# Kernel optimization log

Measured on AMD Instinct MI355X. Metric: run time of the kernel, lower is better.

## Reference

```python
import jax, jax.numpy as jnp
import numpy as np

EMB = 256
HID = 512
VOCAB = 32000
SRC_LEN = 50
TRG_LEN = 50
BATCH = 64


def lstm_layer(x, h0, c0, Wih, Whh, b):
    """x: [T,B,in]; h0,c0: [B,H]; Wih: [4H,in]; Whh: [4H,H]; b: [4H].
    PyTorch gate order i,f,g,o. Returns (ys [T,B,H], hT, cT)."""
    def step(carry, xt):
        h, c = carry
        g = xt @ Wih.T + h @ Whh.T + b
        i, f, gg, o = jnp.split(g, 4, axis=-1)
        c = jax.nn.sigmoid(f) * c + jax.nn.sigmoid(i) * jnp.tanh(gg)
        h = jax.nn.sigmoid(o) * jnp.tanh(c)
        return (h, c), h
    (hT, cT), ys = jax.lax.scan(step, (h0, c0), x)
    return ys, hT, cT


def setup_inputs() -> dict:
    key = jax.random.key(0)
    ks = jax.random.split(key, 20)
    s = 0.05
    d = {
        'src': jax.random.randint(ks[0], (SRC_LEN, BATCH), 0, VOCAB),
        'trg': jax.random.randint(ks[1], (TRG_LEN, BATCH), 0, VOCAB),
        'enc_emb': jax.random.normal(ks[2], (VOCAB, EMB), jnp.float32) * s,
        'enc_Wih0': jax.random.normal(ks[3], (4 * HID, EMB), jnp.float32) * s,
        'enc_Whh0': jax.random.normal(ks[4], (4 * HID, HID), jnp.float32) * s,
        'enc_b0': jnp.zeros((4 * HID,), jnp.float32),
        'enc_Wih1': jax.random.normal(ks[5], (4 * HID, HID), jnp.float32) * s,
        'enc_Whh1': jax.random.normal(ks[6], (4 * HID, HID), jnp.float32) * s,
        'enc_b1': jnp.zeros((4 * HID,), jnp.float32),
        'dec_emb': jax.random.normal(ks[7], (VOCAB, EMB), jnp.float32) * s,
        'dec_Wih0': jax.random.normal(ks[8], (4 * HID, EMB), jnp.float32) * s,
        'dec_Whh0': jax.random.normal(ks[9], (4 * HID, HID), jnp.float32) * s,
        'dec_b0': jnp.zeros((4 * HID,), jnp.float32),
        'dec_Wih1': jax.random.normal(ks[10], (4 * HID, HID), jnp.float32) * s,
        'dec_Whh1': jax.random.normal(ks[11], (4 * HID, HID), jnp.float32) * s,
        'dec_b1': jnp.zeros((4 * HID,), jnp.float32),
        'out_W': jax.random.normal(ks[12], (VOCAB, HID), jnp.float32) * s,
        'out_b': jnp.zeros((VOCAB,), jnp.float32),
    }
    return d


def reference(src, trg, enc_emb, enc_Wih0, enc_Whh0, enc_b0, enc_Wih1, enc_Whh1,
              enc_b1, dec_emb, dec_Wih0, dec_Whh0, dec_b0, dec_Wih1, dec_Whh1,
              dec_b1, out_W, out_b):
    B = src.shape[1]
    z = jnp.zeros((B, HID), enc_emb.dtype)
    # Encoder: 2-layer LSTM over src, keep final (h, c) per layer
    xe = enc_emb[src]                                   # [S,B,E]
    y0, h0, c0 = lstm_layer(xe, z, z, enc_Wih0, enc_Whh0, enc_b0)
    _, h1, c1 = lstm_layer(y0, z, z, enc_Wih1, enc_Whh1, enc_b1)
    # Decoder with teacher forcing: inputs are trg[0:T-1]
    xd = dec_emb[trg[:-1]]                              # [T-1,B,E]
    d0, _, _ = lstm_layer(xd, h0, c0, dec_Wih0, dec_Whh0, dec_b0)
    d1, _, _ = lstm_layer(d0, h1, c1, dec_Wih1, dec_Whh1, dec_b1)
    preds = d1 @ out_W.T + out_b                        # [T-1,B,V]
    return preds
```

## Files before the change

### kernel.cpp

```cpp
#include <hip/hip_runtime.h>
#include <hip/hip_bf16.h>

#define BATCH 64
#define HID 512
#define EMB 256
#define VOCAB 32000
#define G4 2048

typedef __attribute__((ext_vector_type(8))) short short8;
typedef __attribute__((ext_vector_type(4))) float f32x4;
typedef __attribute__((ext_vector_type(4))) unsigned short ush4;

__global__ __launch_bounds__(256) void zero_kernel(float* p, int n){
    int i = blockIdx.x*256 + threadIdx.x;
    if (i < n) p[i] = 0.f;
}

__device__ __forceinline__ unsigned short bf16_rne(float x){
    unsigned b = __float_as_uint(x);
    return (unsigned short)((b + 0x7fffu + ((b >> 16) & 1u)) >> 16);
}
__device__ __forceinline__ void split2(float x, unsigned short& h, unsigned short& l){
    h = bf16_rne(x);
    l = bf16_rne(x - __uint_as_float((unsigned)h << 16));
}

__global__ __launch_bounds__(256) void embed_kernel(const int* __restrict__ tok,
                                                    const float* __restrict__ emb,
                                                    float* __restrict__ out, int T){
    int i = blockIdx.x*256 + threadIdx.x;
    int n = T*BATCH*(EMB/4);
    if (i >= n) return;
    int e4 = i % (EMB/4);
    int tb = i / (EMB/4);
    int id = tok[tb];
    reinterpret_cast<float4*>(out)[(size_t)tb*(EMB/4) + e4] =
        reinterpret_cast<const float4*>(emb + (size_t)id*EMB)[e4];
}

__global__ __launch_bounds__(256) void embed_plane_kernel(const int* __restrict__ tok,
                                                          const float* __restrict__ emb,
                                                          unsigned short* __restrict__ hi,
                                                          unsigned short* __restrict__ lo, int T){
    int i = blockIdx.x*256 + threadIdx.x;
    int n = T*BATCH*(EMB/4);
    if (i >= n) return;
    int e4 = i % (EMB/4);
    int tb = i / (EMB/4);
    int id = tok[tb];
    f32x4 v = reinterpret_cast<const f32x4*>(emb + (size_t)id*EMB)[e4];
    ush4 h, l;
    #pragma unroll
    for (int j = 0; j < 4; j++){ unsigned short a,b; split2(v[j], a, b); h[j]=a; l[j]=b; }
    reinterpret_cast<ush4*>(hi)[(size_t)tb*(EMB/4) + e4] = h;
    reinterpret_cast<ush4*>(lo)[(size_t)tb*(EMB/4) + e4] = l;
}

__global__ __launch_bounds__(256) void split_kernel(const float* __restrict__ in,
                                                    unsigned short* __restrict__ hi,
                                                    unsigned short* __restrict__ lo, int n4){
    int i = blockIdx.x*256 + threadIdx.x;
    if (i >= n4) return;
    f32x4 v = reinterpret_cast<const f32x4*>(in)[i];
    ush4 h, l;
    #pragma unroll
    for (int j = 0; j < 4; j++){ unsigned short a,b; split2(v[j], a, b); h[j]=a; l[j]=b; }
    reinterpret_cast<ush4*>(hi)[i] = h;
    reinterpret_cast<ush4*>(lo)[i] = l;
}

__global__ __launch_bounds__(256) void split_all_kernel(
    const float* __restrict__ outW, unsigned short* __restrict__ Whi,
    const float* __restrict__ w0, unsigned short* __restrict__ w0h, unsigned short* __restrict__ w0l,
    const float* __restrict__ w1, unsigned short* __restrict__ w1h, unsigned short* __restrict__ w1l,
    const float* __restrict__ w2, unsigned short* __restrict__ w2h, unsigned short* __restrict__ w2l,
    const float* __restrict__ w3, unsigned short* __restrict__ w3h, unsigned short* __restrict__ w3l)
{
    int i = blockIdx.x*256 + threadIdx.x;
    if (i < 4096000){
        f32x4 v = reinterpret_cast<const f32x4*>(outW)[i];
        ush4 h;
        #pragma unroll
        for (int j = 0; j < 4; j++) h[j] = bf16_rne(v[j]);
        reinterpret_cast<ush4*>(Whi)[i] = h;
        return;
    }
    i -= 4096000;
    const float* src; unsigned short* dh; unsigned short* dl;
    if (i < 131072){ src = w0; dh = w0h; dl = w0l; }
    else if (i < 131072+262144){ i -= 131072; src = w1; dh = w1h; dl = w1l; }
    else if (i < 131072+262144+131072){ i -= 131072+262144; src = w2; dh = w2h; dl = w2l; }
    else if (i < 131072+262144+131072+262144){ i -= 131072+262144+131072; src = w3; dh = w3h; dl = w3l; }
    else return;
    f32x4 v = reinterpret_cast<const f32x4*>(src)[i];
    ush4 h, l;
    #pragma unroll
    for (int j = 0; j < 4; j++){ unsigned short a,b; split2(v[j], a, b); h[j]=a; l[j]=b; }
    reinterpret_cast<ush4*>(dh)[i] = h;
    reinterpret_cast<ush4*>(dl)[i] = l;
}

template<int KDIM, int NDIM>
__global__ __launch_bounds__(256) void gemm_mfma_split(
    const float* __restrict__ A, const float* __restrict__ B,
    const float* __restrict__ bias, float* __restrict__ C, int M)
{
    constexpr int LS = 40;
    __shared__ unsigned short Ah[128*LS], Al[128*LS], Bh[128*LS], Bl[128*LS];
    const int n0 = blockIdx.x*128, m0 = blockIdx.y*128;
    const int tid  = threadIdx.x;
    const int lane = tid & 63, wid = tid >> 6;
    const int wm = wid >> 1, wn = wid & 1;
    const int srow = tid >> 1, sk = (tid & 1)*16;
    f32x4 acc[4][4] = {};

    for (int k0 = 0; k0 < KDIM; k0 += 32){
        __syncthreads();
        {
            int ar = m0 + srow;
            float xv[16];
            if (ar < M){
                const float4* ap = reinterpret_cast<const float4*>(A + (size_t)ar*KDIM + k0 + sk);
                #pragma unroll
                for (int q = 0; q < 4; q++){
                    float4 v = ap[q];
                    xv[q*4+0]=v.x; xv[q*4+1]=v.y; xv[q*4+2]=v.z; xv[q*4+3]=v.w;
                }
            } else {
                #pragma unroll
                for (int q = 0; q < 16; q++) xv[q] = 0.f;
            }
            #pragma unroll
            for (int q = 0; q < 16; q++){
                unsigned short h,l; split2(xv[q], h, l);
                Ah[srow*LS + sk + q] = h;
                Al[srow*LS + sk + q] = l;
            }
        }
        {
            int br = n0 + srow;
            const float4* bp = reinterpret_cast<const float4*>(B + (size_t)br*KDIM + k0 + sk);
            #pragma unroll
            for (int q = 0; q < 4; q++){
                float4 v = bp[q];
                float xs[4] = {v.x, v.y, v.z, v.w};
                #pragma unroll
                for (int j = 0; j < 4; j++){
                    unsigned short h,l; split2(xs[j], h, l);
                    Bh[srow*LS + sk + q*4 + j] = h;
                    Bl[srow*LS + sk + q*4 + j] = l;
                }
            }
        }
        __syncthreads();
        const int fr = lane & 15, fk = (lane >> 4)*8;
        short8 a_h[4], a_l[4], b_h[4], b_l[4];
        #pragma unroll
        for (int mi = 0; mi < 4; mi++){
            int row = wm*64 + mi*16 + fr;
            a_h[mi] = *reinterpret_cast<const short8*>(&Ah[row*LS + fk]);
            a_l[mi] = *reinterpret_cast<const short8*>(&Al[row*LS + fk]);
        }
        #pragma unroll
        for (int nj = 0; nj < 4; nj++){
            int rowb = wn*64 + nj*16 + fr;
            b_h[nj] = *reinterpret_cast<const short8*>(&Bh[rowb*LS + fk]);
            b_l[nj] = *reinterpret_cast<const short8*>(&Bl[rowb*LS + fk]);
        }
        #pragma unroll
        for (int mi = 0; mi < 4; mi++)
            #pragma unroll
            for (int nj = 0; nj < 4; nj++){
                acc[mi][nj] = __builtin_amdgcn_mfma_f32_16x16x32_bf16(a_h[mi], b_h[nj], acc[mi][nj], 0,0,0);
                acc[mi][nj] = __builtin_amdgcn_mfma_f32_16x16x32_bf16(a_h[mi], b_l[nj], acc[mi][nj], 0,0,0);
                acc[mi][nj] = __builtin_amdgcn_mfma_f32_16x16x32_bf16(a_l[mi], b_h[nj], acc[mi][nj], 0,0,0);
            }
    }
    const int fr = lane & 15, fq = lane >> 4;
    #pragma unroll
    for (int nj = 0; nj < 4; nj++){
        int col = n0 + wn*64 + nj*16 + fr;
        float bv = bias[col];
        #pragma unroll
        for (int mi = 0; mi < 4; mi++){
            int rbase = m0 + wm*64 + mi*16 + fq*4;
            #pragma unroll
            for (int j = 0; j < 4; j++){
                int row = rbase + j;
                if (row < M)
                    __builtin_nontemporal_store(acc[mi][nj][j] + bv, &C[(size_t)row*NDIM + col]);
            }
        }
    }
}

__device__ __forceinline__ void gll16(const unsigned short* g, unsigned short* l){
    __builtin_amdgcn_global_load_lds(
        (const __attribute__((address_space(1))) unsigned int*)g,
        (__attribute__((address_space(3))) unsigned int*)l, 16, 0, 0);
}

template<int KDIM, int NDIM, int NTN>
__device__ __forceinline__ void gemm_gll_body(
    const unsigned short* __restrict__ Ahi, const unsigned short* __restrict__ Alo,
    const unsigned short* __restrict__ Bhi, const unsigned short* __restrict__ Blo,
    const float* __restrict__ bias, float* __restrict__ C, int M,
    int bid_raw, int total)
{
    __shared__ unsigned short P[4][128*32];
    const int q = total >> 3, r8 = total & 7;
    const int xcd = bid_raw & 7, idx = bid_raw >> 3;
    const int lid = (xcd < r8 ? xcd*(q+1) : r8*(q+1) + (xcd - r8)*q) + idx;
    const int m0 = (lid / NTN)*128, n0 = (lid % NTN)*128;

    const int tid  = threadIdx.x;
    const int lane = tid & 63, wid = tid >> 6;
    const int wm = wid >> 1, wn = wid & 1;

    const unsigned short* gsrc = (wid == 0) ? Ahi : (wid == 1) ? Alo
                               : (wid == 2) ? Bhi : Blo;
    const int row0 = (wid < 2) ? m0 : n0;
    const unsigned short* gbase = gsrc + (size_t)(row0 + (lane >> 2))*KDIM
                                       + 8*((lane & 3) ^ ((lane >> 3) & 3));
    unsigned short* lbase = &P[wid][0];

    f32x4 acc[4][4] = {};

    for (int k0 = 0; k0 < KDIM; k0 += 32){
        __syncthreads();
        #pragma unroll
        for (int i = 0; i < 8; i++)
            gll16(gbase + k0 + (size_t)i*16*KDIM, lbase + i*512);
        __syncthreads();

        const int fr = lane & 15, fkq = lane >> 4;
        const int swz = 8*(fkq ^ ((fr >> 1) & 3));
        short8 a_h[4], a_l[4], b_h[4], b_l[4];
        #pragma unroll
        for (int mi = 0; mi < 4; mi++){
            int row = wm*64 + mi*16 + fr;
            a_h[mi] = *reinterpret_cast<const short8*>(&P[0][row*32 + swz]);
            a_l[mi] = *reinterpret_cast<const short8*>(&P[1][row*32 + swz]);
        }
        #pragma unroll
        for (int nj = 0; nj < 4; nj++){
            int row = wn*64 + nj*16 + fr;
            b_h[nj] = *reinterpret_cast<const short8*>(&P[2][row*32 + swz]);
            b_l[nj] = *reinterpret_cast<const short8*>(&P[3][row*32 + swz]);
        }
        #pragma unroll
        for (int mi = 0; mi < 4; mi++)
            #pragma unroll
            for (int nj = 0; nj < 4; nj++){
                acc[mi][nj] = __builtin_amdgcn_mfma_f32_16x16x32_bf16(a_h[mi], b_h[nj], acc[mi][nj], 0,0,0);
                acc[mi][nj] = __builtin_amdgcn_mfma_f32_16x16x32_bf16(a_l[mi], b_h[nj], acc[mi][nj], 0,0,0);
                acc[mi][nj] = __builtin_amdgcn_mfma_f32_16x16x32_bf16(a_h[mi], b_l[nj], acc[mi][nj], 0,0,0);
            }
    }
    const int fr = lane & 15, fq = lane >> 4;
    #pragma unroll
    for (int nj = 0; nj < 4; nj++){
        int col = n0 + wn*64 + nj*16 + fr;
        float bv = bias[col];
        #pragma unroll
        for (int mi = 0; mi < 4; mi++){
            int rbase = m0 + wm*64 + mi*16 + fq*4;
            #pragma unroll
            for (int j = 0; j < 4; j++){
                int row = rbase + j;
                if (row < M)
                    __builtin_nontemporal_store(acc[mi][nj][j] + bv, &C[(size_t)row*NDIM + col]);
            }
        }
    }
}

template<int KDIM, int NDIM, int NTN>
__global__ __launch_bounds__(256) void gemm_planes_gll(
    const unsigned short* Ahi, const unsigned short* Alo,
    const unsigned short* Bhi, const unsigned short* Blo,
    const float* bias, float* C, int M)
{
    gemm_gll_body<KDIM, NDIM, NTN>(Ahi, Alo, Bhi, Blo, bias, C, M,
                                   blockIdx.x, gridDim.x);
}

template<int KDIM, int NDIM, int NTN>
__global__ __launch_bounds__(512) void gemm_planes_256w8(
    const unsigned short* __restrict__ Ahi,
    const unsigned short* __restrict__ Bhi,
    const float* __restrict__ bias, float* __restrict__ C, int M)
{
    __shared__ unsigned short Ah[256*32];
    __shared__ unsigned short Bh[128*32];
    const int total = gridDim.x;
    const int q = total >> 3, r8 = total & 7;
    const int xcd = blockIdx.x & 7, idx = blockIdx.x >> 3;
    const int lid = (xcd < r8 ? xcd*(q+1) : r8*(q+1) + (xcd - r8)*q) + idx;
    const int m0 = (lid / NTN)*256, n0 = (lid % NTN)*128;

    const int tid  = threadIdx.x;
    const int lane = tid & 63, wid = tid >> 6;
    const int wm = wid >> 1, wn = wid & 1;

    const bool stager = (wid < 6);
    const unsigned short* gsrc = (wid < 4) ? Ahi : Bhi;
    const int grow0 = (wid < 4) ? (m0 + wid*64) : (n0 + (wid - 4)*64);
    const unsigned short* gbase = gsrc + (size_t)(grow0 + (lane >> 2))*KDIM
                                       + 8*((lane & 3) ^ ((lane >> 3) & 3));
    unsigned short* lbase = (wid < 4) ? (Ah + wid*64*32) : (Bh + (wid - 4)*64*32);

    f32x4 acc[4][4] = {};

    for (int k0 = 0; k0 < KDIM; k0 += 32){
        __syncthreads();
        if (stager){
            #pragma unroll
            for (int i = 0; i < 4; i++)
                gll16(gbase + k0 + (size_t)i*16*KDIM, lbase + i*512);
        }
        __syncthreads();

        const int fr = lane & 15, fkq = lane >> 4;
        const int swz = 8*(fkq ^ ((fr >> 1) & 3));
        short8 a_h[4], b_h[4];
        #pragma unroll
        for (int nj = 0; nj < 4; nj++){
            int row = wn*64 + nj*16 + fr;
            b_h[nj] = *reinterpret_cast<const short8*>(&Bh[row*32 + swz]);
        }
        #pragma unroll
        for (int mi = 0; mi < 4; mi++){
            int row = wm*64 + mi*16 + fr;
            a_h[mi] = *reinterpret_cast<const short8*>(&Ah[row*32 + swz]);
        }
        #pragma unroll
        for (int mi = 0; mi < 4; mi++)
            #pragma unroll
            for (int nj = 0; nj < 4; nj++)
                acc[mi][nj] = __builtin_amdgcn_mfma_f32_16x16x32_bf16(a_h[mi], b_h[nj], acc[mi][nj], 0,0,0);
    }
    const int fr = lane & 15, fq = lane >> 4;
    #pragma unroll
    for (int nj = 0; nj < 4; nj++){
        int col = n0 + wn*64 + nj*16 + fr;
        float bv = bias[col];
        #pragma unroll
        for (int mi = 0; mi < 4; mi++){
            int rbase = m0 + wm*64 + mi*16 + fq*4;
            #pragma unroll
            for (int j = 0; j < 4; j++){
                int row = rbase + j;
                if (row < M)
                    __builtin_nontemporal_store(acc[mi][nj][j] + bv, &C[(size_t)row*NDIM + col]);
            }
        }
    }
}

__device__ __forceinline__ void lstm_body(
    const float* __restrict__ Xp, const float* __restrict__ Whh,
    const float* __restrict__ hinit, const float* __restrict__ cinit,
    float* __restrict__ ys, float* __restrict__ cfin,
    int T, unsigned* __restrict__ flagbase, int bx,
    unsigned short* __restrict__ phi, unsigned short* __restrict__ plo)
{
    constexpr int WS = 520;
    __shared__ unsigned short hH[8*WS], hL[8*WS];
    __shared__ __align__(16) float red[4*544 + 128];
    __shared__ unsigned short zbuf[8];

    const int bc  = bx & 7, hc = bx >> 3;
    const int hid0 = hc*16;
    const int tid = threadIdx.x;
    const int lane = tid & 63, kc = tid >> 6;
    const int fr = lane & 15, fkq = lane >> 4;
    unsigned* myflag = flagbase + (size_t)(bc*32 + hc)*16;

    if (tid < 8) zbuf[tid] = 0;

    short8 ah[4][4], al[4][4];
    #pragma unroll
    for (int m = 0; m < 4; m++){
        const float* wr = Whh + (size_t)(m*HID + hid0 + fr)*HID;
        #pragma unroll
        for (int s = 0; s < 4; s++){
            int k0 = kc*128 + s*32 + fkq*8;
            f32x4 v0 = *reinterpret_cast<const f32x4*>(wr + k0);
            f32x4 v1 = *reinterpret_cast<const f32x4*>(wr + k0 + 4);
            short8 h8, l8;
            float xv[8] = {v0[0],v0[1],v0[2],v0[3],v1[0],v1[1],v1[2],v1[3]};
            #pragma unroll
            for (int j = 0; j < 8; j++){
                unsigned short hh, ll; split2(xv[j], hh, ll);
                h8[j] = (short)hh; l8[j] = (short)ll;
            }
            ah[m][s] = h8; al[m][s] = l8;
        }
    }

    const int ub = tid >> 4;
    const int uh = tid & 15;
    float creg = 0.f;
    if (tid < 128) creg = cinit[(size_t)(bc*8 + ub)*HID + hid0 + uh];

    const size_t hbase = (size_t)bc*8*HID;
    const float* xprow = Xp + (size_t)(bc*8 + ub)*G4 + hid0 + uh;

    float xn0=0.f, xn1=0.f, xn2=0.f, xn3=0.f;
    if (tid < 128){
        const float* xpr = xprow;
        xn0 = xpr[0]; xn1 = xpr[512]; xn2 = xpr[1024]; xn3 = xpr[1536];
    }

    for (int t = 0; t < T; t++){
        {
            const f32x4* hsrc = reinterpret_cast<const f32x4*>(
                (t == 0) ? (hinit + hbase) : (ys + (size_t)(t-1)*BATCH*HID + hbase));
            #pragma unroll
            for (int j = 0; j < 4; j++){
                int fidx = tid + j*256;
                f32x4 v = hsrc[fidx];
                int e   = fidx*4;
                int row = e >> 9, col = e & 511;
                ush4 h, l;
                #pragma unroll
                for (int qq = 0; qq < 4; qq++){ unsigned short a,b; split2(v[qq], a, b); h[qq]=a; l[qq]=b; }
                *reinterpret_cast<ush4*>(&hH[row*WS + col]) = h;
                *reinterpret_cast<ush4*>(&hL[row*WS + col]) = l;
            }
        }
        __syncthreads();

        {
            f32x4 acc4[4] = {};
            const bool breal = fr < 8;
            #pragma unroll
            for (int s = 0; s < 4; s++){
                int k0 = kc*128 + s*32 + fkq*8;
                short8 bh = breal ? *reinterpret_cast<const short8*>(&hH[fr*WS + k0])
                                  : *reinterpret_cast<const short8*>(zbuf);
                short8 bl = breal ? *reinterpret_cast<const short8*>(&hL[fr*WS + k0])
                                  : *reinterpret_cast<const short8*>(zbuf);
                #pragma unroll
                for (int m = 0; m < 4; m++){
                    acc4[m] = __builtin_amdgcn_mfma_f32_16x16x32_bf16(ah[m][s], bh, acc4[m], 0,0,0);
                    acc4[m] = __builtin_amdgcn_mfma_f32_16x16x32_bf16(ah[m][s], bl, acc4[m], 0,0,0);
                    acc4[m] = __builtin_amdgcn_mfma_f32_16x16x32_bf16(al[m][s], bh, acc4[m], 0,0,0);
                }
            }
            const int b = lane & 15;
            if (b < 8){
                #pragma unroll
                for (int m = 0; m < 4; m++)
                    *reinterpret_cast<f32x4*>(&red[kc*544 + b*68 + m*16 + (lane >> 4)*4]) = acc4[m];
            }
        }
        __syncthreads();

        if (tid < 64){
            #pragma unroll
            for (int b = 0; b < 8; b++)
                red[b*68 + tid] = red[b*68 + tid] + red[544 + b*68 + tid]
                               + red[1088 + b*68 + tid] + red[1632 + b*68 + tid];
        }
        __syncthreads();

        if (tid < 128){
            float gi = red[ub*68 + 0*16 + uh] + xn0;
            float gf = red[ub*68 + 1*16 + uh] + xn1;
            float gg = red[ub*68 + 2*16 + uh] + xn2;
            float go = red[ub*68 + 3*16 + uh] + xn3;
            float si = 1.f/(1.f + expf(-gi));
            float sf = 1.f/(1.f + expf(-gf));
            float so = 1.f/(1.f + expf(-go));
            float tg = tanhf(gg);
            float c = sf*creg + si*tg;
            creg = c;
            float hval = so * tanhf(c);
            red[2176 + tid] = hval;
            if (phi){
                unsigned short hh, ll; split2(hval, hh, ll);
                size_t poff = (size_t)t*BATCH*HID + (size_t)(bc*8 + ub)*HID + hid0 + uh;
                phi[poff] = hh; plo[poff] = ll;
            }
            if (t < T-1){
                const float* xpr = xprow + (size_t)(t+1)*BATCH*G4;
                xn0 = xpr[0]; xn1 = xpr[512]; xn2 = xpr[1024]; xn3 = xpr[1536];
            }
        }
        __syncthreads();

        if (tid < 64){
            if (tid < 32){
                f32x4 v = *reinterpret_cast<const f32x4*>(&red[2176 + tid*4]);
                const f32x4* addr = reinterpret_cast<const f32x4*>(
                    ys + (size_t)t*BATCH*HID
                       + (size_t)(bc*8 + (tid >> 2))*HID + hid0 + (tid & 3)*4);
                asm volatile("global_store_dwordx4 %0, %1, off sc0 sc1"
                             :: "v"(addr), "v"(v) : "memory");
            }
            if (t < T-1){
                asm volatile("s_waitcnt vmcnt(0)" ::: "memory");
                if (tid == 0)
                    __hip_atomic_store(myflag, (unsigned)(t+1),
                                       __ATOMIC_RELAXED, __HIP_MEMORY_SCOPE_AGENT);
                const unsigned tgt = (unsigned)(t+1);
                unsigned* fp = flagbase + (size_t)(bc*32 + (tid & 31))*16;
                unsigned spins = 0;
                bool done = false;
                while (!done && spins < (1u<<20)){
                    unsigned v = tgt;
                    if (tid < 32)
                        v = __hip_atomic_load(fp, __ATOMIC_RELAXED, __HIP_MEMORY_SCOPE_AGENT);
                    done = (bool)__all((int)(v >= tgt));
                    spins++;
                }
            }
        }
        __syncthreads();
    }

    if (tid < 128)
        cfin[(size_t)(bc*8 + ub)*HID + hid0 + uh] = creg;
}

__global__ __launch_bounds__(256, 2) void lstm_layer_k(
    const float* Xp, const float* Whh, const float* hinit, const float* cinit,
    float* ys, float* cfin, int T, unsigned* flagbase,
    unsigned short* phi, unsigned short* plo)
{
    lstm_body(Xp, Whh, hinit, cinit, ys, cfin, T, flagbase, blockIdx.x, phi, plo);
}

__global__ __launch_bounds__(256, 2) void lstm_dual_k(
    const float* Xp0, const float* Whh0, const float* hi0, const float* ci0,
    float* ys0, float* cf0, int T0, unsigned* fl0,
    unsigned short* phi0, unsigned short* plo0,
    const float* Xp1, const float* Whh1, const float* hi1, const float* ci1,
    float* ys1, float* cf1, int T1, unsigned* fl1,
    unsigned short* phi1, unsigned short* plo1)
{
    const int role = blockIdx.x >> 8;
    const int bx = blockIdx.x & 255;
    if (role == 0)
        lstm_body(Xp0, Whh0, hi0, ci0, ys0, cf0, T0, fl0, bx, phi0, plo0);
    else
        lstm_body(Xp1, Whh1, hi1, ci1, ys1, cf1, T1, fl1, bx, phi1, plo1);
}

__global__ __launch_bounds__(256, 2) void lstm_gemm_k(
    const float* Xp, const float* Whh, const float* hinit, const float* cinit,
    float* ys, float* cfin, int T, unsigned* flagbase,
    unsigned short* phi, unsigned short* plo,
    const unsigned short* gAhi, const unsigned short* gAlo,
    const unsigned short* gBhi, const unsigned short* gBlo,
    const float* gbias, float* gC, int gM, int gTotal)
{
    if ((int)blockIdx.x < 256)
        lstm_body(Xp, Whh, hinit, cinit, ys, cfin, T, flagbase, blockIdx.x, phi, plo);
    else
        gemm_gll_body<EMB, G4, 16>(gAhi, gAlo, gBhi, gBlo, gbias, gC, gM,
                                   blockIdx.x - 256, gTotal);
}

extern "C" void kernel_launch(void* const* d_in, const int* in_sizes, int n_in,
                              void* d_out, int out_size, void* d_ws, size_t ws_size,
                              hipStream_t stream) {
    const int*   src      = (const int*)  d_in[0];
    const int*   trg      = (const int*)  d_in[1];
    const float* enc_emb  = (const float*)d_in[2];
    const float* enc_Wih0 = (const float*)d_in[3];
    const float* enc_Whh0 = (const float*)d_in[4];
    const float* enc_b0   = (const float*)d_in[5];
    const float* enc_Wih1 = (const float*)d_in[6];
    const float* enc_Whh1 = (const float*)d_in[7];
    const float* enc_b1   = (const float*)d_in[8];
    const float* dec_emb  = (const float*)d_in[9];
    const float* dec_Wih0 = (const float*)d_in[10];
    const float* dec_Whh0 = (const float*)d_in[11];
    const float* dec_b0   = (const float*)d_in[12];
    const float* dec_Wih1 = (const float*)d_in[13];
    const float* dec_Whh1 = (const float*)d_in[14];
    const float* dec_b1   = (const float*)d_in[15];
    const float* out_W    = (const float*)d_in[16];
    const float* out_b    = (const float*)d_in[17];

    float* ob = (float*)d_out;
    float* Xp   = ob;
    float* xe   = ob + (size_t)6553600;
    float* xd   = ob + (size_t)7372800;
    float* eys0 = ob + (size_t)8175616;
    float* eys1 = ob + (size_t)9814016;
    float* dys0 = ob + (size_t)11452416;
    float* Xp2  = ob + (size_t)13058048;

    float* ws = (float*)d_ws;
    float* dys1 = ws;
    float* c0   = ws + (size_t)1605632;
    float* c1   = ws + (size_t)1638400;
    float* hz   = ws + (size_t)1671168;
    unsigned* flags = (unsigned*)(ws + (size_t)1703936);
    unsigned short* Whi = (unsigned short*)(ws + (size_t)1720320);
    unsigned short* Wlo = Whi + (size_t)16384000;
    unsigned short* Ahi = Wlo + (size_t)16384000;
    unsigned short* Alo = Ahi + (size_t)1703936;
    unsigned short* eW0h = Alo  + (size_t)1703936;
    unsigned short* eW0l = eW0h + (size_t)524288;
    unsigned short* eW1h = eW0l + (size_t)524288;
    unsigned short* eW1l = eW1h + (size_t)1048576;
    unsigned short* dW0h = eW1l + (size_t)1048576;
    unsigned short* dW0l = dW0h + (size_t)524288;
    unsigned short* dW1h = dW0l + (size_t)524288;
    unsigned short* dW1l = dW1h + (size_t)1048576;
    unsigned short* XAh  = dW1l + (size_t)1048576;
    unsigned short* XAl  = XAh  + (size_t)1638400;
    const size_t end_xp = (size_t)1720320*4 +
        2*((size_t)16384000*2 + (size_t)1703936*2 + (size_t)524288*4 +
           (size_t)1048576*4 + (size_t)1638400*2);
    const bool xp_ok = (ws_size >= end_xp);

    {
        int n = 3*BATCH*HID + 4*4096;
        zero_kernel<<<(n+255)/256, 256, 0, stream>>>(c0, n);
    }

    if (xp_ok){
        split_all_kernel<<<(4882432 + 255)/256, 256, 0, stream>>>(
            out_W, Whi,
            enc_Wih0, eW0h, eW0l,  enc_Wih1, eW1h, eW1l,
            dec_Wih0, dW0h, dW0l,  dec_Wih1, dW1h, dW1l);
        embed_plane_kernel<<<(50*BATCH*(EMB/4)+255)/256, 256, 0, stream>>>(src, enc_emb, XAh, XAl, 50);
        embed_plane_kernel<<<(49*BATCH*(EMB/4)+255)/256, 256, 0, stream>>>(trg, dec_emb, Ahi, Alo, 49);
    } else {
        embed_kernel<<<(50*BATCH*(EMB/4)+255)/256, 256, 0, stream>>>(src, enc_emb, xe, 50);
        embed_kernel<<<(49*BATCH*(EMB/4)+255)/256, 256, 0, stream>>>(trg, dec_emb, xd, 49);
    }

    dim3 xgrid(G4/128, 25);

    if (xp_ok)
        gemm_planes_gll<EMB, G4, 16><<<400, 256, 0, stream>>>(XAh, XAl, eW0h, eW0l, enc_b0, Xp, 3200);
    else
        gemm_mfma_split<EMB, G4><<<xgrid, 256, 0, stream>>>(xe, enc_Wih0, enc_b0, Xp, 3200);

    if (xp_ok){
        lstm_gemm_k<<<656, 256, 0, stream>>>(
            Xp, enc_Whh0, hz, hz, eys0, c0, 50, flags + 0, XAh, XAl,
            Ahi, Alo, dW0h, dW0l, dec_b0, Xp2, 3136, 400);
    } else {
        lstm_layer_k<<<256, 256, 0, stream>>>(Xp, enc_Whh0, hz, hz, eys0, c0, 50, flags + 0,
                                              nullptr, nullptr);
        gemm_mfma_split<EMB, G4><<<xgrid, 256, 0, stream>>>(xd, dec_Wih0, dec_b0, Xp2, 3136);
    }

    if (xp_ok)
        gemm_planes_gll<HID, G4, 16><<<400, 256, 0, stream>>>(XAh, XAl, eW1h, eW1l, enc_b1, Xp, 3200);
    else
        gemm_mfma_split<HID, G4><<<xgrid, 256, 0, stream>>>(eys0, enc_Wih1, enc_b1, Xp, 3200);

    lstm_dual_k<<<512, 256, 0, stream>>>(
        Xp,  enc_Whh1, hz,                          hz, eys1, c1, 50, flags + 4096,  nullptr, nullptr,
        Xp2, dec_Whh0, eys0 + (size_t)49*BATCH*HID, c0, dys0, c0, 49, flags + 8192,
        xp_ok ? XAh : nullptr, XAl);

    if (xp_ok)
        gemm_planes_gll<HID, G4, 16><<<400, 256, 0, stream>>>(XAh, XAl, dW1h, dW1l, dec_b1, Xp, 3136);
    else
        gemm_mfma_split<HID, G4><<<xgrid, 256, 0, stream>>>(dys0, dec_Wih1, dec_b1, Xp, 3136);
    lstm_layer_k<<<256, 256, 0, stream>>>(Xp, dec_Whh1, eys1 + (size_t)49*BATCH*HID, c1,
                                          dys1, c1, 49, flags + 12288,
                                          xp_ok ? Ahi : nullptr, Alo);

    if (xp_ok){
        gemm_planes_256w8<HID, VOCAB, 250><<<13*250, 512, 0, stream>>>(
            Ahi, Whi, out_b, (float*)d_out, 3136);
    } else {
        gemm_mfma_split<HID, VOCAB><<<dim3(VOCAB/128, 25), 256, 0, stream>>>(
            dys1, out_W, out_b, (float*)d_out, 3136);
    }
}
```

Measured before the change: 945.8 us.

## Fuse final decoder LSTM layer with vocab projection GEMM via progress flags

Merges the last decoder LSTM layer and the output vocabulary GEMM into one persistent launch. LSTM blocks publish per-batch-chunk progress counters, and GEMM blocks spin-wait until the time steps covering their row tile are done, so the large projection overlaps the serial recurrence. A 512-thread LSTM body variant is added, and the decoder layer-1 input projection gets its own workspace buffer so it does not alias. This relies on co-residency of the LSTM blocks and uses bounded spin loops whose timeouts could break correctness if the GEMM blocks starve the LSTM blocks.

```diff
diff --git a/kernel.cpp b/kernel.cpp
--- a/kernel.cpp
+++ b/kernel.cpp
@@ -56,19 +56,6 @@
     reinterpret_cast<ush4*>(lo)[(size_t)tb*(EMB/4) + e4] = l;
 }
 
-__global__ __launch_bounds__(256) void split_kernel(const float* __restrict__ in,
-                                                    unsigned short* __restrict__ hi,
-                                                    unsigned short* __restrict__ lo, int n4){
-    int i = blockIdx.x*256 + threadIdx.x;
-    if (i >= n4) return;
-    f32x4 v = reinterpret_cast<const f32x4*>(in)[i];
-    ush4 h, l;
-    #pragma unroll
-    for (int j = 0; j < 4; j++){ unsigned short a,b; split2(v[j], a, b); h[j]=a; l[j]=b; }
-    reinterpret_cast<ush4*>(hi)[i] = h;
-    reinterpret_cast<ush4*>(lo)[i] = l;
-}
-
 __global__ __launch_bounds__(256) void split_all_kernel(
     const float* __restrict__ outW, unsigned short* __restrict__ Whi,
     const float* __restrict__ w0, unsigned short* __restrict__ w0h, unsigned short* __restrict__ w0l,
@@ -286,22 +273,39 @@
 }
 
 template<int KDIM, int NDIM, int NTN>
-__global__ __launch_bounds__(512) void gemm_planes_256w8(
+__device__ __forceinline__ void gemm_final_body(
     const unsigned short* __restrict__ Ahi,
     const unsigned short* __restrict__ Bhi,
-    const float* __restrict__ bias, float* __restrict__ C, int M)
+    const float* __restrict__ bias, float* __restrict__ C, int M,
+    int bid, int total, unsigned* __restrict__ gprog, int T)
 {
     __shared__ unsigned short Ah[256*32];
     __shared__ unsigned short Bh[128*32];
-    const int total = gridDim.x;
     const int q = total >> 3, r8 = total & 7;
-    const int xcd = blockIdx.x & 7, idx = blockIdx.x >> 3;
+    const int xcd = bid & 7, idx = bid >> 3;
     const int lid = (xcd < r8 ? xcd*(q+1) : r8*(q+1) + (xcd - r8)*q) + idx;
     const int m0 = (lid / NTN)*256, n0 = (lid % NTN)*128;
 
     const int tid  = threadIdx.x;
     const int lane = tid & 63, wid = tid >> 6;
     const int wm = wid >> 1, wn = wid & 1;
+
+    if (gprog){
+        int thresh = 4*(lid / NTN) + 4;
+        if (thresh > T) thresh = T;
+        if (tid < 64){
+            unsigned spins = 0; bool done = false;
+            while (!done && spins < (1u<<14)){
+                unsigned v = (unsigned)thresh;
+                if (tid < 8)
+                    v = __hip_atomic_load(&gprog[tid], __ATOMIC_RELAXED, __HIP_MEMORY_SCOPE_AGENT);
+                done = (bool)__all((int)(v >= (unsigned)thresh));
+                spins++;
+                if (!done) __builtin_amdgcn_s_sleep(8);
+            }
+        }
+        __syncthreads();
+    }
 
     const bool stager = (wid < 6);
     const unsigned short* gsrc = (wid < 4) ? Ahi : Bhi;
@@ -356,6 +360,15 @@
             }
         }
     }
+}
+
+template<int KDIM, int NDIM, int NTN>
+__global__ __launch_bounds__(512) void gemm_planes_256w8(
+    const unsigned short* Ahi, const unsigned short* Bhi,
+    const float* bias, float* C, int M)
+{
+    gemm_final_body<KDIM, NDIM, NTN>(Ahi, Bhi, bias, C, M,
+                                     blockIdx.x, gridDim.x, nullptr, 0);
 }
 
 __device__ __forceinline__ void lstm_body(
@@ -562,6 +575,217 @@
     else
         gemm_gll_body<EMB, G4, 16>(gAhi, gAlo, gBhi, gBlo, gbias, gC, gM,
                                    blockIdx.x - 256, gTotal);
+}
+
+__device__ __forceinline__ void lstm_body8(
+    const float* __restrict__ Xp, const float* __restrict__ Whh,
+    const float* __restrict__ hinit, const float* __restrict__ cinit,
+    float* __restrict__ ys, float* __restrict__ cfin,
+    int T, unsigned* __restrict__ flagbase, int bx,
+    unsigned short* __restrict__ phi, unsigned short* __restrict__ plo,
+    unsigned* __restrict__ gprog)
+{
+    constexpr int WS = 520;
+    __shared__ unsigned short hH[8*WS], hL[8*WS];
+    __shared__ __align__(16) float red[8*544 + 128];
+    __shared__ unsigned short zbuf[8];
+
+    const int bc = bx & 7, hc = bx >> 3;
+    const int hid0 = hc*16;
+    const int tid = threadIdx.x;
+    const int lane = tid & 63, kc = tid >> 6;
+    const int fr = lane & 15, fkq = lane >> 4;
+    unsigned* myflag = flagbase + (size_t)(bc*32 + hc)*16;
+
+    if (tid < 8) zbuf[tid] = 0;
+
+    short8 ah[4][2], al[4][2];
+    #pragma unroll
+    for (int m = 0; m < 4; m++){
+        const float* wr = Whh + (size_t)(m*HID + hid0 + fr)*HID;
+        #pragma unroll
+        for (int s = 0; s < 2; s++){
+            int k0 = kc*64 + s*32 + fkq*8;
+            f32x4 v0 = *reinterpret_cast<const f32x4*>(wr + k0);
+            f32x4 v1 = *reinterpret_cast<const f32x4*>(wr + k0 + 4);
+            short8 h8, l8;
+            float xv[8] = {v0[0],v0[1],v0[2],v0[3],v1[0],v1[1],v1[2],v1[3]};
+            #pragma unroll
+            for (int j = 0; j < 8; j++){
+                unsigned short hh, ll; split2(xv[j], hh, ll);
+                h8[j] = (short)hh; l8[j] = (short)ll;
+            }
+            ah[m][s] = h8; al[m][s] = l8;
+        }
+    }
+
+    const int ub = tid >> 4;
+    const int uh = tid & 15;
+    float creg = 0.f;
+    if (tid < 128) creg = cinit[(size_t)(bc*8 + ub)*HID + hid0 + uh];
+
+    const size_t hbase = (size_t)bc*8*HID;
+    const float* xprow = Xp + (size_t)(bc*8 + ub)*G4 + hid0 + uh;
+
+    float xn0=0.f, xn1=0.f, xn2=0.f, xn3=0.f;
+    if (tid < 128){
+        const float* xpr = xprow;
+        xn0 = xpr[0]; xn1 = xpr[512]; xn2 = xpr[1024]; xn3 = xpr[1536];
+    }
+
+    for (int t = 0; t < T; t++){
+        {
+            const f32x4* hsrc = reinterpret_cast<const f32x4*>(
+                (t == 0) ? (hinit + hbase) : (ys + (size_t)(t-1)*BATCH*HID + hbase));
+            #pragma unroll
+            for (int j = 0; j < 2; j++){
+                int fidx = tid + j*512;
+                f32x4 v = hsrc[fidx];
+                int e   = fidx*4;
+                int row = e >> 9, col = e & 511;
+                ush4 h, l;
+                #pragma unroll
+                for (int qq = 0; qq < 4; qq++){ unsigned short a,b; split2(v[qq], a, b); h[qq]=a; l[qq]=b; }
+                *reinterpret_cast<ush4*>(&hH[row*WS + col]) = h;
+                *reinterpret_cast<ush4*>(&hL[row*WS + col]) = l;
+            }
+        }
+        __syncthreads();
+
+        {
+            f32x4 acc4[4] = {};
+            const bool breal = fr < 8;
+            #pragma unroll
+            for (int s = 0; s < 2; s++){
+                int k0 = kc*64 + s*32 + fkq*8;
+                short8 bh = breal ? *reinterpret_cast<const short8*>(&hH[fr*WS + k0])
+                                  : *reinterpret_cast<const short8*>(zbuf);
+                short8 bl = breal ? *reinterpret_cast<const short8*>(&hL[fr*WS + k0])
+                                  : *reinterpret_cast<const short8*>(zbuf);
+                #pragma unroll
+                for (int m = 0; m < 4; m++){
+                    acc4[m] = __builtin_amdgcn_mfma_f32_16x16x32_bf16(ah[m][s], bh, acc4[m], 0,0,0);
+                    acc4[m] = __builtin_amdgcn_mfma_f32_16x16x32_bf16(ah[m][s], bl, acc4[m], 0,0,0);
+                    acc4[m] = __builtin_amdgcn_mfma_f32_16x16x32_bf16(al[m][s], bh, acc4[m], 0,0,0);
+                }
+            }
+            const int b = lane & 15;
+            if (b < 8){
+                #pragma unroll
+                for (int m = 0; m < 4; m++)
+                    *reinterpret_cast<f32x4*>(&red[kc*544 + b*68 + m*16 + (lane >> 4)*4]) = acc4[m];
+            }
+        }
+        __syncthreads();
+
+        if (tid < 64){
+            #pragma unroll
+            for (int b = 0; b < 8; b++){
+                float v = red[b*68 + tid];
+                #pragma unroll
+                for (int s = 1; s < 8; s++) v += red[s*544 + b*68 + tid];
+                red[b*68 + tid] = v;
+            }
+        }
+        __syncthreads();
+
+        if (tid < 128){
+            float gi = red[ub*68 + 0*16 + uh] + xn0;
+            float gf = red[ub*68 + 1*16 + uh] + xn1;
+            float gg = red[ub*68 + 2*16 + uh] + xn2;
+            float go = red[ub*68 + 3*16 + uh] + xn3;
+            float si = 1.f/(1.f + expf(-gi));
+            float sf = 1.f/(1.f + expf(-gf));
+            float so = 1.f/(1.f + expf(-go));
+            float tg = tanhf(gg);
+            float c = sf*creg + si*tg;
+            creg = c;
+            red[4352 + tid] = so * tanhf(c);
+            if (t < T-1){
+                const float* xpr = xprow + (size_t)(t+1)*BATCH*G4;
+                xn0 = xpr[0]; xn1 = xpr[512]; xn2 = xpr[1024]; xn3 = xpr[1536];
+            }
+        }
+        __syncthreads();
+
+        if (tid < 64){
+            if (tid < 32){
+                f32x4 v = *reinterpret_cast<const f32x4*>(&red[4352 + tid*4]);
+                size_t eoff = (size_t)t*BATCH*HID
+                            + (size_t)(bc*8 + (tid >> 2))*HID + hid0 + (tid & 3)*4;
+                const f32x4* addr = reinterpret_cast<const f32x4*>(ys + eoff);
+                asm volatile("global_store_dwordx4 %0, %1, off sc0 sc1"
+                             :: "v"(addr), "v"(v) : "memory");
+                if (phi){
+                    ush4 hh, ll;
+                    #pragma unroll
+                    for (int j = 0; j < 4; j++){ unsigned short a,b; split2(v[j], a, b); hh[j]=a; ll[j]=b; }
+                    const ush4* pa = reinterpret_cast<const ush4*>(phi + eoff);
+                    const ush4* pb = reinterpret_cast<const ush4*>(plo + eoff);
+                    asm volatile("global_store_dwordx2 %0, %1, off sc0 sc1"
+                                 :: "v"(pa), "v"(hh) : "memory");
+                    asm volatile("global_store_dwordx2 %0, %1, off sc0 sc1"
+                                 :: "v"(pb), "v"(ll) : "memory");
+                }
+            }
+            asm volatile("s_waitcnt vmcnt(0)" ::: "memory");
+            if (tid == 0)
+                __hip_atomic_store(myflag, (unsigned)(t+1),
+                                   __ATOMIC_RELAXED, __HIP_MEMORY_SCOPE_AGENT);
+            if (t < T-1){
+                const unsigned tgt = (unsigned)(t+1);
+                unsigned* fp = flagbase + (size_t)(bc*32 + (tid & 31))*16;
+                unsigned spins = 0;
+                bool done = false;
+                while (!done && spins < (1u<<20)){
+                    unsigned v = tgt;
+                    if (tid < 32)
+                        v = __hip_atomic_load(fp, __ATOMIC_RELAXED, __HIP_MEMORY_SCOPE_AGENT);
+                    done = (bool)__all((int)(v >= tgt));
+                    spins++;
+                }
+                if (gprog && hc == 0 && tid == 0)
+                    __hip_atomic_store(&gprog[bc], tgt,
+                                       __ATOMIC_RELAXED, __HIP_MEMORY_SCOPE_AGENT);
+            }
+        }
+        __syncthreads();
+    }
+
+    if (tid < 128)
+        cfin[(size_t)(bc*8 + ub)*HID + hid0 + uh] = creg;
+
+    if (gprog && hc == 0 && tid < 64){
+        const unsigned tgt = (unsigned)T;
+        unsigned* fp = flagbase + (size_t)(bc*32 + (tid & 31))*16;
+        unsigned spins = 0;
+        bool done = false;
+        while (!done && spins < (1u<<20)){
+            unsigned v = tgt;
+            if (tid < 32)
+                v = __hip_atomic_load(fp, __ATOMIC_RELAXED, __HIP_MEMORY_SCOPE_AGENT);
+            done = (bool)__all((int)(v >= tgt));
+            spins++;
+        }
+        if (tid == 0)
+            __hip_atomic_store(&gprog[bc], tgt,
+                               __ATOMIC_RELAXED, __HIP_MEMORY_SCOPE_AGENT);
+    }
+}
+
+__global__ __launch_bounds__(512, 2) void lstm_final_k(
+    const float* Xp, const float* Whh, const float* hinit, const float* cinit,
+    float* ys, float* cfin, int T, unsigned* flagbase,
+    unsigned short* phi, unsigned short* plo, unsigned* gprog,
+    const unsigned short* gA, const unsigned short* gB,
+    const float* gbias, float* gC, int gM, int gTotal)
+{
+    if ((int)blockIdx.x < 256)
+        lstm_body8(Xp, Whh, hinit, cinit, ys, cfin, T, flagbase, blockIdx.x,
+                   phi, plo, gprog);
+    else
+        gemm_final_body<HID, VOCAB, 250>(gA, gB, gbias, gC, gM,
+                                         blockIdx.x - 256, gTotal, gprog, T);
 }
 
 extern "C" void kernel_launch(void* const* d_in, const int* in_sizes, int n_in,
@@ -601,6 +825,7 @@
     float* c1   = ws + (size_t)1638400;
     float* hz   = ws + (size_t)1671168;
     unsigned* flags = (unsigned*)(ws + (size_t)1703936);
+    unsigned* gprog = ((unsigned*)(ws + (size_t)1703936)) - 16;
     unsigned short* Whi = (unsigned short*)(ws + (size_t)1720320);
     unsigned short* Wlo = Whi + (size_t)16384000;
     unsigned short* Ahi = Wlo + (size_t)16384000;
@@ -618,7 +843,10 @@
     const size_t end_xp = (size_t)1720320*4 +
         2*((size_t)16384000*2 + (size_t)1703936*2 + (size_t)524288*4 +
            (size_t)1048576*4 + (size_t)1638400*2);
-    const bool xp_ok = (ws_size >= end_xp);
+    float* Xp3 = (float*)((char*)d_ws + end_xp);
+    const size_t end_fused = end_xp + (size_t)3136*2048*4;
+    const bool xp_ok    = (ws_size >= end_xp);
+    const bool fused_ok = (ws_size >= end_fused);
 
     {
         int n = 3*BATCH*HID + 4*4096;
@@ -664,18 +892,25 @@
         Xp2, dec_Whh0, eys0 + (size_t)49*BATCH*HID, c0, dys0, c0, 49, flags + 8192,
         xp_ok ? XAh : nullptr, XAl);
 
+    float* XpD1 = fused_ok ? Xp3 : Xp;
     if (xp_ok)
-        gemm_planes_gll<HID, G4, 16><<<400, 256, 0, stream>>>(XAh, XAl, dW1h, dW1l, dec_b1, Xp, 3136);
+        gemm_planes_gll<HID, G4, 16><<<400, 256, 0, stream>>>(XAh, XAl, dW1h, dW1l, dec_b1, XpD1, 3136);
     else
-        gemm_mfma_split<HID, G4><<<xgrid, 256, 0, stream>>>(dys0, dec_Wih1, dec_b1, Xp, 3136);
-    lstm_layer_k<<<256, 256, 0, stream>>>(Xp, dec_Whh1, eys1 + (size_t)49*BATCH*HID, c1,
-                                          dys1, c1, 49, flags + 12288,
-                                          xp_ok ? Ahi : nullptr, Alo);
-
-    if (xp_ok){
+        gemm_mfma_split<HID, G4><<<xgrid, 256, 0, stream>>>(dys0, dec_Wih1, dec_b1, XpD1, 3136);
+
+    if (fused_ok){
+        lstm_final_k<<<256 + 3250, 512, 0, stream>>>(
+            Xp3, dec_Whh1, eys1 + (size_t)49*BATCH*HID, c1, dys1, c1, 49, flags + 12288,
+            Ahi, Alo, gprog,
+            Ahi, Whi, out_b, (float*)d_out, 3136, 3250);
+    } else if (xp_ok){
+        lstm_layer_k<<<256, 256, 0, stream>>>(XpD1, dec_Whh1, eys1 + (size_t)49*BATCH*HID, c1,
+                                              dys1, c1, 49, flags + 12288, Ahi, Alo);
         gemm_planes_256w8<HID, VOCAB, 250><<<13*250, 512, 0, stream>>>(
             Ahi, Whi, out_b, (float*)d_out, 3136);
     } else {
+        lstm_layer_k<<<256, 256, 0, stream>>>(XpD1, dec_Whh1, eys1 + (size_t)49*BATCH*HID, c1,
+                                              dys1, c1, 49, flags + 12288, nullptr, nullptr);
         gemm_mfma_split<HID, VOCAB><<<dim3(VOCAB/128, 25), 256, 0, stream>>>(
             dys1, out_W, out_b, (float*)d_out, 3136);
     }
```

Result: slower. 996.2 us (+5.3%).
